# Kernel optimization log

Hardware: AMD Instinct MI355X
Metric: run time of the kernel (lower is better)

Reference implementation:

```python
import jax, jax.numpy as jnp
import numpy as np

N_NODES = 100000
N_EDGES = 1600000
DIM = 64


def setup_inputs() -> dict:
    key = jax.random.key(0)
    ks = jax.random.split(key, 10)
    return {
        "h_real": jax.random.normal(ks[0], (N_NODES, DIM), dtype=jnp.float32),
        "h_imag": jax.random.normal(ks[1], (N_NODES, DIM), dtype=jnp.float32),
        "d": jax.random.uniform(ks[2], (N_NODES,), dtype=jnp.float32),
        "w_real": jax.random.normal(ks[3], (N_EDGES,), dtype=jnp.float32),
        "w_imag": jax.random.normal(ks[4], (N_EDGES,), dtype=jnp.float32),
        "src": jax.random.randint(ks[5], (N_EDGES,), 0, N_NODES, dtype=jnp.int32),
        "dst": jax.random.randint(ks[6], (N_EDGES,), 0, N_NODES, dtype=jnp.int32),
        "W1": jax.random.normal(ks[7], (DIM, DIM), dtype=jnp.float32) * (1.414 / np.sqrt(DIM)),
        "b1": jnp.zeros((DIM,), dtype=jnp.float32),
        "W2": jax.random.normal(ks[8], (DIM, DIM), dtype=jnp.float32) * (1.414 / np.sqrt(DIM)),
        "b2": jnp.zeros((DIM,), dtype=jnp.float32),
    }


def reference(h_real, h_imag, d, w_real, w_imag, src, dst, W1, b1, W2, b2):
    n = h_real.shape[0]
    # per-edge complex coefficient e = d_dst * d_src * (w_real + i w_imag)
    dd = d[dst] * d[src]                      # [E]
    e_r = (dd * w_real)[:, None]              # [E,1]
    e_i = (dd * w_imag)[:, None]              # [E,1]
    hr = h_real[src]                          # [E,D]
    hi = h_imag[src]                          # [E,D]
    # complex multiply e * h, fused single pass over edges
    m_r = e_r * hr - e_i * hi                 # [E,D]
    m_i = e_i * hr + e_r * hi                 # [E,D]
    z_real = jax.ops.segment_sum(m_r, dst, num_segments=n)  # [N,D]
    z_imag = jax.ops.segment_sum(m_i, dst, num_segments=n)  # [N,D]
    # note: original overwrites z_real first, then z_imag uses the NEW z_real
    zr = (z_real @ W1.T + b1) - (z_imag @ W2.T + b2)
    zi = (zr @ W2.T + b2) + (z_imag @ W1.T + b1)
    return zr, zi
```

## Files before the change

### kernel.cpp

```cpp
#include <hip/hip_runtime.h>
#include <hip/hip_bf16.h>

#define N_NODES 100000
#define N_EDGES 1600000
#define DIM 64

#define TILE 4096
#define B1 ((N_EDGES + TILE - 1) / TILE)
#define K1 ((N_NODES + 255) / 256)
#define NCOUNTS (K1 * B1)
#define SCAN_BLOCK 1024
#define NSB ((NCOUNTS + SCAN_BLOCK - 1) / SCAN_BLOCK)
#define PACKB ((N_NODES * DIM + 255) / 256)
#define PLACE_CAP 4736

typedef __attribute__((ext_vector_type(8))) short bf16x8;
typedef __attribute__((ext_vector_type(4))) float f32x4;

#if defined(__has_builtin)
#if __has_builtin(__builtin_amdgcn_fdot2_f32_bf16)
#define HAVE_DOT2 1
typedef __attribute__((ext_vector_type(2))) __bf16 bf16x2v;
#endif
#endif


__device__ __forceinline__ unsigned pack_bf16x2(float lo, float hi) {
  unsigned ulo = (unsigned)__hip_bfloat16_raw(__float2bfloat16(lo)).x;
  unsigned uhi = (unsigned)__hip_bfloat16_raw(__float2bfloat16(hi)).x;
  return ulo | (uhi << 16);
}
__device__ __forceinline__ float unpack_lo(unsigned u) {
  return __int_as_float((int)(u << 16));
}
__device__ __forceinline__ float unpack_hi(unsigned u) {
  return __int_as_float((int)(u & 0xFFFF0000u));
}
__device__ __forceinline__ unsigned short f2bf(float x) {
  return __hip_bfloat16_raw(__float2bfloat16(x)).x;
}

__global__ __launch_bounds__(256) void setup_fused_kernel(
    const float* __restrict__ h_real, const float* __restrict__ h_imag,
    unsigned* __restrict__ hpack, const float* __restrict__ W1,
    const float* __restrict__ b1, const float* __restrict__ W2,
    const float* __restrict__ b2, unsigned short* __restrict__ At,
    float* __restrict__ cvec, const int* __restrict__ dst,
    int* __restrict__ counts) {
  const int bid = blockIdx.x;
  const int tid = threadIdx.x;
  if (bid < PACKB) {
    const int i = bid * 256 + tid;
    if (i < N_NODES * DIM) hpack[i] = pack_bf16x2(h_real[i], h_imag[i]);
    return;
  }
  if (bid < PACKB + 64) {
    const int idx = (bid - PACKB) * 256 + tid;
    if (idx < 128 * 128) {
      const int n = idx >> 7, k = idx & 127;
      float v;
      if (n < 64) {
        v = (k < 64) ? W1[n * 64 + k] : -W2[n * 64 + (k - 64)];
      } else {
        const int nn = n - 64;
        if (k < 64) {
          float s = 0.0f;
          for (int j = 0; j < 64; ++j) s += W1[j * 64 + k] * W2[nn * 64 + j];
          v = s;
        } else {
          const int kk = k - 64;
          float s = 0.0f;
          for (int j = 0; j < 64; ++j) s += W2[j * 64 + kk] * W2[nn * 64 + j];
          v = W1[nn * 64 + kk] - s;
        }
      }
      At[n * 128 + k] = f2bf(v);
    }
    if (idx < 128) {
      if (idx < 64) {
        cvec[idx] = b1[idx] - b2[idx];
      } else {
        const int nn = idx - 64;
        float s = 0.0f;
        for (int j = 0; j < 64; ++j) s += (b1[j] - b2[j]) * W2[nn * 64 + j];
        cvec[idx] = s + b1[nn] + b2[nn];
      }
    }
    return;
  }
  __shared__ int lh[K1];
  const int hb = bid - PACKB - 64;
  for (int i = tid; i < K1; i += 256) lh[i] = 0;
  __syncthreads();
  const int e0 = hb * TILE;
  const int e1 = min(e0 + TILE, N_EDGES);
  for (int e = e0 + tid; e < e1; e += 256) atomicAdd(&lh[dst[e] >> 8], 1);
  __syncthreads();
  for (int b = tid; b < K1; b += 256) counts[b * B1 + hb] = lh[b];
}

__global__ __launch_bounds__(SCAN_BLOCK) void scan1_kernel(
    int* __restrict__ cnt, int* __restrict__ bsum) {
  __shared__ int s[SCAN_BLOCK];
  const int tid = threadIdx.x;
  const int i = blockIdx.x * SCAN_BLOCK + tid;
  const int v = (i < NCOUNTS) ? cnt[i] : 0;
  s[tid] = v;
  __syncthreads();
#pragma unroll
  for (int off = 1; off < SCAN_BLOCK; off <<= 1) {
    int t = (tid >= off) ? s[tid - off] : 0;
    __syncthreads();
    s[tid] += t;
    __syncthreads();
  }
  if (i < NCOUNTS) cnt[i] = s[tid] - v;
  if (tid == SCAN_BLOCK - 1) bsum[blockIdx.x] = s[tid];
}

__global__ void scan2_kernel(const int* __restrict__ bsum, int* __restrict__ bpre) {
  if (threadIdx.x == 0 && blockIdx.x == 0) {
    int run = 0;
    for (int b = 0; b < NSB; ++b) {
      bpre[b] = run;
      run += bsum[b];
    }
  }
}

__global__ __launch_bounds__(SCAN_BLOCK) void scan3_kernel(
    int* __restrict__ cnt, const int* __restrict__ bpre) {
  const int i = blockIdx.x * SCAN_BLOCK + threadIdx.x;
  if (i < NCOUNTS) cnt[i] += bpre[blockIdx.x];
}

__global__ __launch_bounds__(512) void partition_kernel(
    const int* __restrict__ src, const int* __restrict__ dst,
    const float* __restrict__ dvec,
    const float* __restrict__ w_real, const float* __restrict__ w_imag,
    const int* __restrict__ coffs, unsigned long long* __restrict__ records) {
  __shared__ unsigned long long stage[TILE];
  __shared__ unsigned short sb[TILE];
  __shared__ int lhist[512];
  __shared__ int lbase[K1];
  __shared__ int lcur[K1];
  __shared__ int gbase[K1];
  const int tid = threadIdx.x;
  const int blk = blockIdx.x;
  const int e0 = blk * TILE;
  const int cnt_t = min(TILE, N_EDGES - e0);

  lhist[tid] = 0;
  __syncthreads();
  for (int j = tid; j < cnt_t; j += 512) atomicAdd(&lhist[dst[e0 + j] >> 8], 1);
  __syncthreads();
  const int myc = lhist[tid];
  __syncthreads();
#pragma unroll
  for (int off = 1; off < 512; off <<= 1) {
    int v = (tid >= off) ? lhist[tid - off] : 0;
    __syncthreads();
    lhist[tid] += v;
    __syncthreads();
  }
  if (tid < K1) {
    const int ex = lhist[tid] - myc;
    lbase[tid] = ex;
    lcur[tid] = ex;
    gbase[tid] = coffs[tid * B1 + blk];
  }
  __syncthreads();

  for (int j = tid; j < cnt_t; j += 512) {
    const int e = e0 + j;
    const int t = dst[e];
    const int s = src[e];
    const int b = t >> 8;
    const float ds = dvec[s];
    const unsigned lo = (unsigned)s | ((unsigned)(t & 255) << 17);
    const unsigned hi = pack_bf16x2(ds * w_real[e], ds * w_imag[e]);
    const int r = atomicAdd(&lcur[b], 1);
    stage[r] = ((unsigned long long)hi << 32) | lo;
    sb[r] = (unsigned short)b;
  }
  __syncthreads();
  for (int i = tid; i < cnt_t; i += 512) {
    const int b = sb[i];
    records[gbase[b] + (i - lbase[b])] = stage[i];
  }
}

__global__ __launch_bounds__(256) void place_kernel(
    unsigned long long* __restrict__ records, const int* __restrict__ coffs,
    int* __restrict__ inc) {
  const int b = blockIdx.x;
  const int tid = threadIdx.x;
  const int bstart = coffs[b * B1];
  const int bend = (b == K1 - 1) ? N_EDGES : coffs[(b + 1) * B1];
  const int cnt = min(bend - bstart, PLACE_CAP);
  const int nbase = b << 8;
  const int nn = min(256, N_NODES - nbase);

  __shared__ unsigned long long stage[PLACE_CAP];
  __shared__ int ncnt[256];
  __shared__ int ncur[256];

  ncnt[tid] = 0;
  __syncthreads();
  for (int i = tid; i < cnt; i += 256) {
    const unsigned long long rec = records[bstart + i];
    stage[i] = rec;
    atomicAdd(&ncnt[((unsigned)rec >> 17) & 255], 1);
  }
  __syncthreads();
  const int myc = ncnt[tid];
  __syncthreads();
#pragma unroll
  for (int off = 1; off < 256; off <<= 1) {
    int v = (tid >= off) ? ncnt[tid - off] : 0;
    __syncthreads();
    ncnt[tid] += v;
    __syncthreads();
  }
  const int base = bstart + ncnt[tid] - myc;
  ncur[tid] = base;
  if (tid < nn) inc[nbase + tid] = base + myc;
  __syncthreads();
  for (int i = tid; i < cnt; i += 256) {
    const unsigned long long rec = stage[i];
    const int pos = atomicAdd(&ncur[((unsigned)rec >> 17) & 255], 1);
    records[pos] = rec;
  }
}

__global__ __launch_bounds__(1024) void pull_fused_kernel(
    const uint2* __restrict__ records, const int* __restrict__ inc,
    const float* __restrict__ dvec, const unsigned* __restrict__ hpack,
    const unsigned short* __restrict__ At, const float* __restrict__ cvec,
    float* __restrict__ zr_out, float* __restrict__ zi_out) {
  __shared__ unsigned short zs[16][136];
  const int lane = threadIdx.x & 63;
  const int wave = threadIdx.x >> 6;
  const int node0 = blockIdx.x * 16;
  const int n = node0 + wave;

  const int start = (n == 0) ? 0 : inc[n - 1];
  const int end = inc[n];
  const unsigned* __restrict__ hl = hpack + lane;

  float sr = 0.0f, si = 0.0f;
  int p = start;
#if HAVE_DOT2
#define ACC(RR, HH)                                                     \
  {                                                                     \
    const unsigned wneg = RR.y ^ 0x80000000u;             \
    const unsigned wswp = (RR.y >> 16) | (RR.y << 16);    \
    const bf16x2v hv = __builtin_bit_cast(bf16x2v, HH);                 \
    sr = __builtin_amdgcn_fdot2_f32_bf16(__builtin_bit_cast(bf16x2v, wneg), \
                                         hv, sr, false);                \
    si = __builtin_amdgcn_fdot2_f32_bf16(__builtin_bit_cast(bf16x2v, wswp), \
                                         hv, si, false);                \
  }
#else
#define ACC(RR, HH)                                                     \
  {                                                                     \
    const float er = unpack_lo(RR.y), ei = unpack_hi(RR.y);             \
    const float hr = unpack_lo(HH), hi = unpack_hi(HH);                 \
    sr += er * hr - ei * hi;                                            \
    si += ei * hr + er * hi;                                            \
  }
#endif
  for (; p + 4 <= end; p += 4) {
    const uint2 r0 = records[p + 0];
    const uint2 r1 = records[p + 1];
    const uint2 r2 = records[p + 2];
    const uint2 r3 = records[p + 3];
    const unsigned h0 = hl[(size_t)(r0.x & 0x1FFFF) * DIM];
    const unsigned h1 = hl[(size_t)(r1.x & 0x1FFFF) * DIM];
    const unsigned h2 = hl[(size_t)(r2.x & 0x1FFFF) * DIM];
    const unsigned h3 = hl[(size_t)(r3.x & 0x1FFFF) * DIM];
    ACC(r0, h0) ACC(r1, h1) ACC(r2, h2) ACC(r3, h3)
  }
  for (; p < end; ++p) {
    const uint2 r0 = records[p];
    const unsigned h0 = hl[(size_t)(r0.x & 0x1FFFF) * DIM];
    ACC(r0, h0)
  }
#undef ACC

  const float dn = dvec[n];
  zs[wave][lane] = f2bf(dn * sr);
  zs[wave][64 + lane] = f2bf(dn * si);
  __syncthreads();

  if (wave < 8) {
    const int t = wave;
    const int m = lane & 15;
    const int q = lane >> 4;

    bf16x8 a[4];
#pragma unroll
    for (int c = 0; c < 4; ++c)
      a[c] = *reinterpret_cast<const bf16x8*>(&zs[m][c * 32 + q * 8]);

    f32x4 acc = (f32x4){0.f, 0.f, 0.f, 0.f};
    const unsigned short* brow = At + (size_t)(t * 16 + m) * 128 + q * 8;
#pragma unroll
    for (int c = 0; c < 4; ++c) {
      bf16x8 bfrag = *reinterpret_cast<const bf16x8*>(brow + c * 32);
      acc = __builtin_amdgcn_mfma_f32_16x16x32_bf16(a[c], bfrag, acc, 0, 0, 0);
    }

    const int nf = t * 16 + m;
    const float bias = cvec[nf];
    float* outp = (nf < 64) ? zr_out : zi_out;
    const int nn = nf & 63;
#pragma unroll
    for (int r = 0; r < 4; ++r) {
      const int node = node0 + q * 4 + r;
      outp[(size_t)node * 64 + nn] = acc[r] + bias;
    }
  }
}

extern "C" void kernel_launch(void* const* d_in, const int* in_sizes, int n_in,
                              void* d_out, int out_size, void* d_ws, size_t ws_size,
                              hipStream_t stream) {
  const float* h_real = (const float*)d_in[0];
  const float* h_imag = (const float*)d_in[1];
  const float* dvec   = (const float*)d_in[2];
  const float* w_real = (const float*)d_in[3];
  const float* w_imag = (const float*)d_in[4];
  const int*   src    = (const int*)d_in[5];
  const int*   dst    = (const int*)d_in[6];
  const float* W1     = (const float*)d_in[7];
  const float* b1     = (const float*)d_in[8];
  const float* W2     = (const float*)d_in[9];
  const float* b2     = (const float*)d_in[10];

  char* ws = (char*)d_ws;
  unsigned short* At = (unsigned short*)ws;
  float* cvec = (float*)(ws + 128 * 128 * 2);
  unsigned long long* records = (unsigned long long*)(ws + 33792);
  unsigned* hpack = (unsigned*)(ws + 33792 + (size_t)N_EDGES * 8);
  int* counts = (int*)(ws + 33792 + (size_t)N_EDGES * 8 + (size_t)N_NODES * DIM * 4);
  int* bsum = counts + NCOUNTS;
  int* bpre = bsum + NSB;
  int* inc  = bpre + NSB;

  float* zr_out = (float*)d_out;
  float* zi_out = zr_out + (size_t)N_NODES * DIM;

  setup_fused_kernel<<<PACKB + 64 + B1, 256, 0, stream>>>(
      h_real, h_imag, (unsigned*)hpack, W1, b1, W2, b2, At, cvec, dst, counts);
  scan1_kernel<<<NSB, SCAN_BLOCK, 0, stream>>>(counts, bsum);
  scan2_kernel<<<1, 64, 0, stream>>>(bsum, bpre);
  scan3_kernel<<<NSB, SCAN_BLOCK, 0, stream>>>(counts, bpre);
  partition_kernel<<<B1, 512, 0, stream>>>(src, dst, dvec, w_real, w_imag,
                                           counts, records);
  place_kernel<<<K1, 256, 0, stream>>>(records, counts, inc);
  pull_fused_kernel<<<N_NODES / 16, 1024, 0, stream>>>(
      (const uint2*)records, inc, dvec, hpack, At, cvec, zr_out, zi_out);
}
```

Before: 292.4 us.

## Replace count-scan-place pipeline with atomic-cursor fixed-capacity buckets and split epilogue

Drops the histogram, three-stage scan and place kernels. Partition now reserves space in fixed-capacity per-bucket regions through global atomic cursors. A new bucket kernel sorts each bucket's records by node in shared memory, accumulates the messages and writes bf16 z to a scratch buffer placed inside the output. A separate MFMA epilogue kernel then applies the combined linear layers. This removes several launches and a global pass over the records, at the cost of one bucket per block with less parallelism in the pull stage, a round trip of z through memory, and silently dropping edges if a bucket exceeds its capacity.

```diff
diff --git a/kernel.cpp b/kernel.cpp
--- a/kernel.cpp
+++ b/kernel.cpp
@@ -8,11 +8,8 @@
 #define TILE 4096
 #define B1 ((N_EDGES + TILE - 1) / TILE)
 #define K1 ((N_NODES + 255) / 256)
-#define NCOUNTS (K1 * B1)
-#define SCAN_BLOCK 1024
-#define NSB ((NCOUNTS + SCAN_BLOCK - 1) / SCAN_BLOCK)
+#define CAP 4608
 #define PACKB ((N_NODES * DIM + 255) / 256)
-#define PLACE_CAP 4736
 
 typedef __attribute__((ext_vector_type(8))) short bf16x8;
 typedef __attribute__((ext_vector_type(4))) float f32x4;
@@ -45,8 +42,7 @@
     unsigned* __restrict__ hpack, const float* __restrict__ W1,
     const float* __restrict__ b1, const float* __restrict__ W2,
     const float* __restrict__ b2, unsigned short* __restrict__ At,
-    float* __restrict__ cvec, const int* __restrict__ dst,
-    int* __restrict__ counts) {
+    float* __restrict__ cvec) {
   const int bid = blockIdx.x;
   const int tid = threadIdx.x;
   if (bid < PACKB) {
@@ -54,97 +50,50 @@
     if (i < N_NODES * DIM) hpack[i] = pack_bf16x2(h_real[i], h_imag[i]);
     return;
   }
-  if (bid < PACKB + 64) {
-    const int idx = (bid - PACKB) * 256 + tid;
-    if (idx < 128 * 128) {
-      const int n = idx >> 7, k = idx & 127;
-      float v;
-      if (n < 64) {
-        v = (k < 64) ? W1[n * 64 + k] : -W2[n * 64 + (k - 64)];
+  const int idx = (bid - PACKB) * 256 + tid;
+  if (idx < 128 * 128) {
+    const int n = idx >> 7, k = idx & 127;
+    float v;
+    if (n < 64) {
+      v = (k < 64) ? W1[n * 64 + k] : -W2[n * 64 + (k - 64)];
+    } else {
+      const int nn = n - 64;
+      if (k < 64) {
+        float s = 0.0f;
+        for (int j = 0; j < 64; ++j) s += W1[j * 64 + k] * W2[nn * 64 + j];
+        v = s;
       } else {
-        const int nn = n - 64;
-        if (k < 64) {
-          float s = 0.0f;
-          for (int j = 0; j < 64; ++j) s += W1[j * 64 + k] * W2[nn * 64 + j];
-          v = s;
-        } else {
-          const int kk = k - 64;
-          float s = 0.0f;
-          for (int j = 0; j < 64; ++j) s += W2[j * 64 + kk] * W2[nn * 64 + j];
-          v = W1[nn * 64 + kk] - s;
-        }
+        const int kk = k - 64;
+        float s = 0.0f;
+        for (int j = 0; j < 64; ++j) s += W2[j * 64 + kk] * W2[nn * 64 + j];
+        v = W1[nn * 64 + kk] - s;
       }
-      At[n * 128 + k] = f2bf(v);
-    }
-    if (idx < 128) {
-      if (idx < 64) {
-        cvec[idx] = b1[idx] - b2[idx];
-      } else {
-        const int nn = idx - 64;
-        float s = 0.0f;
-        for (int j = 0; j < 64; ++j) s += (b1[j] - b2[j]) * W2[nn * 64 + j];
-        cvec[idx] = s + b1[nn] + b2[nn];
-      }
-    }
-    return;
-  }
-  __shared__ int lh[K1];
-  const int hb = bid - PACKB - 64;
-  for (int i = tid; i < K1; i += 256) lh[i] = 0;
-  __syncthreads();
-  const int e0 = hb * TILE;
-  const int e1 = min(e0 + TILE, N_EDGES);
-  for (int e = e0 + tid; e < e1; e += 256) atomicAdd(&lh[dst[e] >> 8], 1);
-  __syncthreads();
-  for (int b = tid; b < K1; b += 256) counts[b * B1 + hb] = lh[b];
-}
-
-__global__ __launch_bounds__(SCAN_BLOCK) void scan1_kernel(
-    int* __restrict__ cnt, int* __restrict__ bsum) {
-  __shared__ int s[SCAN_BLOCK];
-  const int tid = threadIdx.x;
-  const int i = blockIdx.x * SCAN_BLOCK + tid;
-  const int v = (i < NCOUNTS) ? cnt[i] : 0;
-  s[tid] = v;
-  __syncthreads();
-#pragma unroll
-  for (int off = 1; off < SCAN_BLOCK; off <<= 1) {
-    int t = (tid >= off) ? s[tid - off] : 0;
-    __syncthreads();
-    s[tid] += t;
-    __syncthreads();
-  }
-  if (i < NCOUNTS) cnt[i] = s[tid] - v;
-  if (tid == SCAN_BLOCK - 1) bsum[blockIdx.x] = s[tid];
-}
-
-__global__ void scan2_kernel(const int* __restrict__ bsum, int* __restrict__ bpre) {
-  if (threadIdx.x == 0 && blockIdx.x == 0) {
-    int run = 0;
-    for (int b = 0; b < NSB; ++b) {
-      bpre[b] = run;
-      run += bsum[b];
-    }
-  }
-}
-
-__global__ __launch_bounds__(SCAN_BLOCK) void scan3_kernel(
-    int* __restrict__ cnt, const int* __restrict__ bpre) {
-  const int i = blockIdx.x * SCAN_BLOCK + threadIdx.x;
-  if (i < NCOUNTS) cnt[i] += bpre[blockIdx.x];
+    }
+    At[n * 128 + k] = f2bf(v);
+  }
+  if (idx < 128) {
+    if (idx < 64) {
+      cvec[idx] = b1[idx] - b2[idx];
+    } else {
+      const int nn = idx - 64;
+      float s = 0.0f;
+      for (int j = 0; j < 64; ++j) s += (b1[j] - b2[j]) * W2[nn * 64 + j];
+      cvec[idx] = s + b1[nn] + b2[nn];
+    }
+  }
 }
 
 __global__ __launch_bounds__(512) void partition_kernel(
     const int* __restrict__ src, const int* __restrict__ dst,
     const float* __restrict__ dvec,
     const float* __restrict__ w_real, const float* __restrict__ w_imag,
-    const int* __restrict__ coffs, unsigned long long* __restrict__ records) {
+    int* __restrict__ cursor, unsigned long long* __restrict__ records) {
   __shared__ unsigned long long stage[TILE];
   __shared__ unsigned short sb[TILE];
   __shared__ int lhist[512];
-  __shared__ int lbase[K1];
-  __shared__ int lcur[K1];
-  __shared__ int gbase[K1];
+  __shared__ int lbase[512];
+  __shared__ int lcur[512];
+  __shared__ int gbase[512];
   const int tid = threadIdx.x;
   const int blk = blockIdx.x;
   const int e0 = blk * TILE;
@@ -163,11 +112,11 @@
     lhist[tid] += v;
     __syncthreads();
   }
-  if (tid < K1) {
+  {
     const int ex = lhist[tid] - myc;
     lbase[tid] = ex;
     lcur[tid] = ex;
-    gbase[tid] = coffs[tid * B1 + blk];
+    gbase[tid] = (tid < K1 && myc > 0) ? atomicAdd(&cursor[tid], myc) : 0;
   }
   __syncthreads();
 
@@ -186,131 +135,154 @@
   __syncthreads();
   for (int i = tid; i < cnt_t; i += 512) {
     const int b = sb[i];
-    records[gbase[b] + (i - lbase[b])] = stage[i];
-  }
-}
-
-__global__ __launch_bounds__(256) void place_kernel(
-    unsigned long long* __restrict__ records, const int* __restrict__ coffs,
-    int* __restrict__ inc) {
+    const int pos = gbase[b] + (i - lbase[b]);
+    if (pos < CAP) records[(size_t)b * CAP + pos] = stage[i];
+  }
+}
+
+__global__ __launch_bounds__(512) void pull_bucket_kernel(
+    const unsigned long long* __restrict__ records, const int* __restrict__ cursor,
+    const float* __restrict__ dvec, const unsigned* __restrict__ hpack,
+    unsigned short* __restrict__ zcat) {
+  __shared__ unsigned long long stage[CAP];
+  __shared__ unsigned short sidx[CAP];
+  __shared__ int ncnt[256];
+  __shared__ int noff[256];
+  __shared__ int ncur[256];
+
+  const int tid = threadIdx.x;
   const int b = blockIdx.x;
-  const int tid = threadIdx.x;
-  const int bstart = coffs[b * B1];
-  const int bend = (b == K1 - 1) ? N_EDGES : coffs[(b + 1) * B1];
-  const int cnt = min(bend - bstart, PLACE_CAP);
-  const int nbase = b << 8;
-  const int nn = min(256, N_NODES - nbase);
-
-  __shared__ unsigned long long stage[PLACE_CAP];
-  __shared__ int ncnt[256];
-  __shared__ int ncur[256];
-
-  ncnt[tid] = 0;
-  __syncthreads();
-  for (int i = tid; i < cnt; i += 256) {
-    const unsigned long long rec = records[bstart + i];
+  const int cnt = min(cursor[b], CAP);
+  const unsigned long long* __restrict__ reg = records + (size_t)b * CAP;
+
+  if (tid < 256) ncnt[tid] = 0;
+  __syncthreads();
+  for (int i = tid; i < cnt; i += 512) {
+    const unsigned long long rec = reg[i];
     stage[i] = rec;
     atomicAdd(&ncnt[((unsigned)rec >> 17) & 255], 1);
   }
   __syncthreads();
-  const int myc = ncnt[tid];
+  int myc = 0;
+  if (tid < 256) {
+    myc = ncnt[tid];
+    noff[tid] = myc;
+  }
   __syncthreads();
 #pragma unroll
   for (int off = 1; off < 256; off <<= 1) {
-    int v = (tid >= off) ? ncnt[tid - off] : 0;
+    int v = 0;
+    if (tid < 256 && tid >= off) v = noff[tid - off];
     __syncthreads();
-    ncnt[tid] += v;
+    if (tid < 256) noff[tid] += v;
     __syncthreads();
   }
-  const int base = bstart + ncnt[tid] - myc;
-  ncur[tid] = base;
-  if (tid < nn) inc[nbase + tid] = base + myc;
-  __syncthreads();
-  for (int i = tid; i < cnt; i += 256) {
-    const unsigned long long rec = stage[i];
-    const int pos = atomicAdd(&ncur[((unsigned)rec >> 17) & 255], 1);
-    records[pos] = rec;
-  }
-}
-
-__global__ __launch_bounds__(1024) void pull_fused_kernel(
-    const uint2* __restrict__ records, const int* __restrict__ inc,
-    const float* __restrict__ dvec, const unsigned* __restrict__ hpack,
-    const unsigned short* __restrict__ At, const float* __restrict__ cvec,
-    float* __restrict__ zr_out, float* __restrict__ zi_out) {
-  __shared__ unsigned short zs[16][136];
+  if (tid < 256) {
+    const int ex = noff[tid] - myc;
+    noff[tid] = ex;
+    ncur[tid] = ex;
+  }
+  __syncthreads();
+  for (int i = tid; i < cnt; i += 512) {
+    const int nl = ((unsigned)stage[i] >> 17) & 255;
+    const int r = atomicAdd(&ncur[nl], 1);
+    sidx[r] = (unsigned short)i;
+  }
+  __syncthreads();
+
+  const int lane = tid & 63;
+  const int wave = tid >> 6;
+  const unsigned* __restrict__ hl = hpack + lane;
+
+  for (int nl = wave; nl < 256; nl += 8) {
+    const int n = (b << 8) + nl;
+    if (n >= N_NODES) break;
+    const int s0 = noff[nl];
+    const int e1 = s0 + ncnt[nl];
+
+    float sr = 0.0f, si = 0.0f;
+    int p = s0;
+#if HAVE_DOT2
+#define ACC(WW, HH)                                                      \
+  {                                                                      \
+    const unsigned wneg = (WW) ^ 0x80000000u;              \
+    const unsigned wswp = ((WW) >> 16) | ((WW) << 16);     \
+    const bf16x2v hv = __builtin_bit_cast(bf16x2v, HH);                  \
+    sr = __builtin_amdgcn_fdot2_f32_bf16(__builtin_bit_cast(bf16x2v, wneg), \
+                                         hv, sr, false);                 \
+    si = __builtin_amdgcn_fdot2_f32_bf16(__builtin_bit_cast(bf16x2v, wswp), \
+                                         hv, si, false);                 \
+  }
+#else
+#define ACC(WW, HH)                                                      \
+  {                                                                      \
+    const float er = unpack_lo(WW), ei = unpack_hi(WW);                  \
+    const float hr = unpack_lo(HH), hi = unpack_hi(HH);                  \
+    sr += er * hr - ei * hi;                                             \
+    si += ei * hr + er * hi;                                             \
+  }
+#endif
+    for (; p + 4 <= e1; p += 4) {
+      const int i0 = sidx[p + 0];
+      const int i1 = sidx[p + 1];
+      const int i2 = sidx[p + 2];
+      const int i3 = sidx[p + 3];
+      const unsigned long long r0 = stage[i0];
+      const unsigned long long r1 = stage[i1];
+      const unsigned long long r2 = stage[i2];
+      const unsigned long long r3 = stage[i3];
+      const unsigned h0 = hl[(size_t)((unsigned)r0 & 0x1FFFF) * DIM];
+      const unsigned h1 = hl[(size_t)((unsigned)r1 & 0x1FFFF) * DIM];
+      const unsigned h2 = hl[(size_t)((unsigned)r2 & 0x1FFFF) * DIM];
+      const unsigned h3 = hl[(size_t)((unsigned)r3 & 0x1FFFF) * DIM];
+      ACC((unsigned)(r0 >> 32), h0)
+      ACC((unsigned)(r1 >> 32), h1)
+      ACC((unsigned)(r2 >> 32), h2)
+      ACC((unsigned)(r3 >> 32), h3)
+    }
+    for (; p < e1; ++p) {
+      const unsigned long long r0 = stage[sidx[p]];
+      const unsigned h0 = hl[(size_t)((unsigned)r0 & 0x1FFFF) * DIM];
+      ACC((unsigned)(r0 >> 32), h0)
+    }
+#undef ACC
+
+    const float dn = dvec[n];
+    zcat[(size_t)n * 128 + lane] = f2bf(dn * sr);
+    zcat[(size_t)n * 128 + 64 + lane] = f2bf(dn * si);
+  }
+}
+
+__global__ __launch_bounds__(256) void mfma_epilogue_kernel(
+    const unsigned short* zcat, const unsigned short* __restrict__ At,
+    const float* __restrict__ cvec, float* zr_out, float* zi_out) {
   const int lane = threadIdx.x & 63;
-  const int wave = threadIdx.x >> 6;
-  const int node0 = blockIdx.x * 16;
-  const int n = node0 + wave;
-
-  const int start = (n == 0) ? 0 : inc[n - 1];
-  const int end = inc[n];
-  const unsigned* __restrict__ hl = hpack + lane;
-
-  float sr = 0.0f, si = 0.0f;
-  int p = start;
-#if HAVE_DOT2
-#define ACC(RR, HH)                                                     \
-  {                                                                     \
-    const unsigned wneg = RR.y ^ 0x80000000u;             \
-    const unsigned wswp = (RR.y >> 16) | (RR.y << 16);    \
-    const bf16x2v hv = __builtin_bit_cast(bf16x2v, HH);                 \
-    sr = __builtin_amdgcn_fdot2_f32_bf16(__builtin_bit_cast(bf16x2v, wneg), \
-                                         hv, sr, false);                \
-    si = __builtin_amdgcn_fdot2_f32_bf16(__builtin_bit_cast(bf16x2v, wswp), \
-                                         hv, si, false);                \
-  }
-#else
-#define ACC(RR, HH)                                                     \
-  {                                                                     \
-    const float er = unpack_lo(RR.y), ei = unpack_hi(RR.y);             \
-    const float hr = unpack_lo(HH), hi = unpack_hi(HH);                 \
-    sr += er * hr - ei * hi;                                            \
-    si += ei * hr + er * hi;                                            \
-  }
-#endif
-  for (; p + 4 <= end; p += 4) {
-    const uint2 r0 = records[p + 0];
-    const uint2 r1 = records[p + 1];
-    const uint2 r2 = records[p + 2];
-    const uint2 r3 = records[p + 3];
-    const unsigned h0 = hl[(size_t)(r0.x & 0x1FFFF) * DIM];
-    const unsigned h1 = hl[(size_t)(r1.x & 0x1FFFF) * DIM];
-    const unsigned h2 = hl[(size_t)(r2.x & 0x1FFFF) * DIM];
-    const unsigned h3 = hl[(size_t)(r3.x & 0x1FFFF) * DIM];
-    ACC(r0, h0) ACC(r1, h1) ACC(r2, h2) ACC(r3, h3)
-  }
-  for (; p < end; ++p) {
-    const uint2 r0 = records[p];
-    const unsigned h0 = hl[(size_t)(r0.x & 0x1FFFF) * DIM];
-    ACC(r0, h0)
-  }
-#undef ACC
-
-  const float dn = dvec[n];
-  zs[wave][lane] = f2bf(dn * sr);
-  zs[wave][64 + lane] = f2bf(dn * si);
-  __syncthreads();
-
-  if (wave < 8) {
-    const int t = wave;
-    const int m = lane & 15;
-    const int q = lane >> 4;
-
-    bf16x8 a[4];
-#pragma unroll
-    for (int c = 0; c < 4; ++c)
-      a[c] = *reinterpret_cast<const bf16x8*>(&zs[m][c * 32 + q * 8]);
-
-    f32x4 acc = (f32x4){0.f, 0.f, 0.f, 0.f};
+  const int tile = blockIdx.x * (blockDim.x >> 6) + (threadIdx.x >> 6);
+  if (tile >= N_NODES / 16) return;
+  const int node0 = tile * 16;
+  const int m = lane & 15;
+  const int q = lane >> 4;
+
+  bf16x8 a[4];
+  const unsigned short* arow = zcat + (size_t)(node0 + m) * 128 + q * 8;
+#pragma unroll
+  for (int c = 0; c < 4; ++c)
+    a[c] = *reinterpret_cast<const bf16x8*>(arow + c * 32);
+
+  f32x4 acc[8];
+#pragma unroll
+  for (int t = 0; t < 8; ++t) {
+    acc[t] = (f32x4){0.f, 0.f, 0.f, 0.f};
     const unsigned short* brow = At + (size_t)(t * 16 + m) * 128 + q * 8;
 #pragma unroll
     for (int c = 0; c < 4; ++c) {
       bf16x8 bfrag = *reinterpret_cast<const bf16x8*>(brow + c * 32);
-      acc = __builtin_amdgcn_mfma_f32_16x16x32_bf16(a[c], bfrag, acc, 0, 0, 0);
-    }
-
+      acc[t] = __builtin_amdgcn_mfma_f32_16x16x32_bf16(a[c], bfrag, acc[t], 0, 0, 0);
+    }
+  }
+
+#pragma unroll
+  for (int t = 0; t < 8; ++t) {
     const int nf = t * 16 + m;
     const float bias = cvec[nf];
     float* outp = (nf < 64) ? zr_out : zi_out;
@@ -318,7 +290,7 @@
 #pragma unroll
     for (int r = 0; r < 4; ++r) {
       const int node = node0 + q * 4 + r;
-      outp[(size_t)node * 64 + nn] = acc[r] + bias;
+      outp[(size_t)node * 64 + nn] = acc[t][r] + bias;
     }
   }
 }
@@ -341,24 +313,23 @@
   char* ws = (char*)d_ws;
   unsigned short* At = (unsigned short*)ws;
   float* cvec = (float*)(ws + 128 * 128 * 2);
-  unsigned long long* records = (unsigned long long*)(ws + 33792);
-  unsigned* hpack = (unsigned*)(ws + 33792 + (size_t)N_EDGES * 8);
-  int* counts = (int*)(ws + 33792 + (size_t)N_EDGES * 8 + (size_t)N_NODES * DIM * 4);
-  int* bsum = counts + NCOUNTS;
-  int* bpre = bsum + NSB;
-  int* inc  = bpre + NSB;
+  unsigned* hpack = (unsigned*)(ws + 33792);
+  int* cursor = (int*)(ws + 33792 + (size_t)N_NODES * DIM * 4);
 
   float* zr_out = (float*)d_out;
   float* zi_out = zr_out + (size_t)N_NODES * DIM;
-
-  setup_fused_kernel<<<PACKB + 64 + B1, 256, 0, stream>>>(
-      h_real, h_imag, (unsigned*)hpack, W1, b1, W2, b2, At, cvec, dst, counts);
-  scan1_kernel<<<NSB, SCAN_BLOCK, 0, stream>>>(counts, bsum);
-  scan2_kernel<<<1, 64, 0, stream>>>(bsum, bpre);
-  scan3_kernel<<<NSB, SCAN_BLOCK, 0, stream>>>(counts, bpre);
+  unsigned long long* records = (unsigned long long*)zr_out;
+  unsigned short* zcat = (unsigned short*)zi_out;
+
+  hipMemsetAsync(cursor, 0, (size_t)K1 * sizeof(int), stream);
+
+  setup_fused_kernel<<<PACKB + 64, 256, 0, stream>>>(h_real, h_imag, hpack, W1,
+                                                     b1, W2, b2, At, cvec);
   partition_kernel<<<B1, 512, 0, stream>>>(src, dst, dvec, w_real, w_imag,
-                                           counts, records);
-  place_kernel<<<K1, 256, 0, stream>>>(records, counts, inc);
-  pull_fused_kernel<<<N_NODES / 16, 1024, 0, stream>>>(
-      (const uint2*)records, inc, dvec, hpack, At, cvec, zr_out, zi_out);
-}
+                                           cursor, records);
+  pull_bucket_kernel<<<K1, 512, 0, stream>>>(records, cursor, dvec, hpack, zcat);
+
+  const int tiles = N_NODES / 16;
+  mfma_epilogue_kernel<<<(tiles + 3) / 4, 256, 0, stream>>>(zcat, At, cvec,
+                                                            zr_out, zi_out);
+}
```

Result: slower. 308.6 us (+5.5%).
